# Kernel tuning notes

Hardware: AMD Instinct MI355X
Metric: run time of the kernel (lower is better)

The kernel has to match this reference:

```python
import jax, jax.numpy as jnp
import numpy as np

B, S, D, H, E, K = 8, 8192, 256, 1024, 8, 2


def setup_inputs() -> dict:
    key = jax.random.key(0)
    ks = jax.random.split(key, 7)
    s_in = 1.0 / np.sqrt(D)
    s_hid = 1.0 / np.sqrt(H)
    return {
        "x": jax.random.normal(ks[0], (B, S, D), dtype=jnp.float32),
        "Wg": jax.random.uniform(ks[1], (E, D), jnp.float32, -s_in, s_in),
        "bg": jax.random.uniform(ks[2], (E,), jnp.float32, -s_in, s_in),
        "W1": jax.random.uniform(ks[3], (E, H, D), jnp.float32, -s_in, s_in),
        "b1": jax.random.uniform(ks[4], (E, H), jnp.float32, -s_in, s_in),
        "W2": jax.random.uniform(ks[5], (E, D, H), jnp.float32, -s_hid, s_hid),
        "b2": jax.random.uniform(ks[6], (E, D), jnp.float32, -s_hid, s_hid),
    }


def reference(x, Wg, bg, W1, b1, W2, b2):
    # gate: [B,S,E]
    gate_scores = jnp.einsum("bsd,ed->bse", x, Wg) + bg
    topk_scores, topk_idx = jax.lax.top_k(gate_scores, K)  # [B,S,K]
    topk_probs = jax.nn.softmax(topk_scores, axis=-1)      # [B,S,K]
    # combine weight per expert: sum over top-k slots of prob * one_hot(idx)
    combine = jnp.sum(topk_probs[..., None] * jax.nn.one_hot(topk_idx, E, dtype=x.dtype), axis=-2)  # [B,S,E]
    out = jnp.zeros_like(x)
    for e in range(E):  # small fixed loop over experts
        h = jax.nn.relu(jnp.einsum("bsd,hd->bsh", x, W1[e]) + b1[e])
        y = jnp.einsum("bsh,dh->bsd", h, W2[e]) + b2[e]
        out = out + combine[..., e:e + 1] * y
    return out
```

## Files before the change

kernel.cpp:

```cpp
#include <hip/hip_runtime.h>
#include <hip/hip_bf16.h>

#define T_TOKENS 65536
#define D_DIM 256
#define H_DIM 1024
#define E_NUM 8
#define MT 128
#define HC 32
#define NCHUNK 32
#define GTB 64

typedef __attribute__((ext_vector_type(4))) float f32x4;
typedef __attribute__((ext_vector_type(8))) short s16x8;
typedef __attribute__((ext_vector_type(4))) unsigned int u32x4;
typedef __attribute__((ext_vector_type(4))) unsigned short u16x4;
typedef __attribute__((address_space(3))) unsigned int lds_u32;
typedef const __attribute__((address_space(1))) unsigned int glb_u32;

#define MFMA __builtin_amdgcn_mfma_f32_16x16x32_bf16

__device__ __forceinline__ unsigned short f2bf(float f){
  union { float f; unsigned u; } v; v.f = f;
  unsigned r = v.u + 0x7FFFu + ((v.u >> 16) & 1u);
  return (unsigned short)(r >> 16);
}
__device__ __forceinline__ float bf2f(unsigned short h){
  return __uint_as_float((unsigned)h << 16);
}
__device__ __forceinline__ unsigned cvtpk(float lo, float hi){
  unsigned r;
  asm("v_cvt_pk_bf16_f32 %0, %1, %2" : "=v"(r) : "v"(lo), "v"(hi));
  return r;
}
__device__ __forceinline__ unsigned long long pack4(f32x4 v){
  return (unsigned long long)f2bf(v.x)
       | ((unsigned long long)f2bf(v.y) << 16)
       | ((unsigned long long)f2bf(v.z) << 32)
       | ((unsigned long long)f2bf(v.w) << 48);
}

__device__ __forceinline__ void cvt_unit(int i, const float* __restrict__ W1,
                                         const float* __restrict__ W2,
                                         char* __restrict__ wsw){
  const int N1 = (E_NUM * H_DIM * D_DIM) / 4;
  unsigned long long pk;
  size_t off;
  if (i < N1){
    pk = pack4(((const f32x4*)W1)[i]);
    int idx = i << 2;
    int e  = idx >> 18;
    int h  = (idx >> 8) & (H_DIM - 1);
    int d0 = idx & (D_DIM - 1);
    int c = h >> 5, mi = (h >> 4) & 1, mrow = h & 15;
    int ks = d0 >> 5, qj = (d0 >> 3) & 3, e2 = d0 & 7;
    off = ((size_t)(e * NCHUNK + c) << 15)
        + (size_t)(((ks*2 + mi) << 10) + ((qj*16 + mrow) << 4) + (e2 << 1));
  } else {
    pk = pack4(((const f32x4*)W2)[i - N1]);
    int idx = (i - N1) << 2;
    int e   = idx >> 18;
    int d   = (idx >> 10) & (D_DIM - 1);
    int h0  = idx & (H_DIM - 1);
    int c   = h0 >> 5;
    int h32 = h0 & 31;
    int mi = (h32 >> 4) & 1, qj = (h32 >> 2) & 3;
    off = ((size_t)(e * NCHUNK + c) << 15) + 16384
        + (size_t)(((d >> 4) << 10) + ((qj * 16 + (d & 15)) << 4) + (mi << 3));
  }
  *(unsigned long long*)(wsw + off) = pk;
}

__global__ __launch_bounds__(256) void gate_kernel(
    const float* __restrict__ x, const float* __restrict__ Wg,
    const float* __restrict__ bg,
    const float* __restrict__ W1, const float* __restrict__ W2,
    char* __restrict__ wsw,
    int* __restrict__ counts, int* __restrict__ tok_ids, float* __restrict__ rrec)
{
  __shared__ int lcnt[E_NUM];
  __shared__ int lbase[E_NUM];
  __shared__ unsigned char aexp[GTB * 2];
  __shared__ short         apos[GTB * 2];

  int tid = threadIdx.x, wave = tid >> 6, lane = tid & 63;

  int gthr = blockIdx.x * 256 + tid;
#pragma unroll
  for (int j = 0; j < 4; ++j)
    cvt_unit(gthr + j * ((T_TOKENS / GTB) * 256), W1, W2, wsw);

  if (tid < E_NUM) lcnt[tid] = 0;
  __syncthreads();

  int t0 = blockIdx.x * GTB;
#pragma unroll 1
  for (int i = 0; i < GTB / 4; ++i){
    int tl = wave * (GTB / 4) + i;
    int t = t0 + tl;
    f32x4 xv = *(const f32x4*)(x + (size_t)t * D_DIM + 4*lane);
    float s[E_NUM];
#pragma unroll
    for (int e = 0; e < E_NUM; ++e){
      f32x4 w = *(const f32x4*)(Wg + e*D_DIM + 4*lane);
      s[e] = xv.x*w.x + xv.y*w.y + xv.z*w.z + xv.w*w.w;
    }
#pragma unroll
    for (int off = 32; off; off >>= 1){
#pragma unroll
      for (int e = 0; e < E_NUM; ++e) s[e] += __shfl_xor(s[e], off);
    }
#pragma unroll
    for (int e = 0; e < E_NUM; ++e) s[e] += bg[e];
    int e0 = 0; float v0 = s[0];
#pragma unroll
    for (int e = 1; e < E_NUM; ++e) if (s[e] > v0){ v0 = s[e]; e0 = e; }
    int e1 = -1; float v1 = -3.4e38f;
#pragma unroll
    for (int e = 0; e < E_NUM; ++e){
      if (e == e0) continue;
      if (s[e] > v1){ v1 = s[e]; e1 = e; }
    }
    float ex = __expf(v1 - v0);
    float inv = 1.f / (1.f + ex);
    float p0 = inv, p1 = ex * inv;
    if (lane == 0){
      int li = tl * 2;
      int pos0 = atomicAdd(&lcnt[e0], 1);
      int pos1 = atomicAdd(&lcnt[e1], 1);
      aexp[li]   = (unsigned char)e0; apos[li]   = (short)pos0;
      aexp[li+1] = (unsigned char)e1; apos[li+1] = (short)pos1;
      f32x4 rr; rr.x = p0; rr.y = p1; rr.z = (float)e0; rr.w = (float)e1;
      *(f32x4*)(rrec + (size_t)t * 4) = rr;
    }
  }
  __syncthreads();
  if (tid < E_NUM) lbase[tid] = atomicAdd(counts + tid*16, lcnt[tid]);
  __syncthreads();
  if (tid < GTB * 2){
    int t = t0 + (tid >> 1);
    int e = aexp[tid];
    int idx = lbase[e] + apos[tid];
    tok_ids[e*T_TOKENS + idx] = t | ((tid & 1) << 16);
  }
}

__global__ __launch_bounds__(256, 2) void ffn_kernel(
  const float* __restrict__ x, const char* __restrict__ wsw,
  const float* __restrict__ b1,
  const int* __restrict__ counts, const int* __restrict__ tok_ids,
  unsigned short* __restrict__ yslot)
{
  const int e    = blockIdx.x & 7;
  const int tile = blockIdx.x >> 3;
  const int cnt  = counts[e * 16];
  const int base = tile * MT;
  if (base >= cnt) return;

  __shared__ __align__(1024) unsigned short W1s[2][8192];
  __shared__ __align__(1024) unsigned short W2h[2][4096];
  __shared__ __align__(16)   float b1s[H_DIM];
  __shared__ int sTok[MT];

  const int tid = threadIdx.x, wave = tid >> 6, lane = tid & 63;
  const int mrow = lane & 15, qj = lane >> 4;
  const char* wexp = wsw + ((size_t)(e * NCHUNK) << 15);

  auto stage_w1 = [&](int c, int buf){
    const char* src = wexp + ((size_t)c << 15);
    char* dst = (char*)&W1s[buf][0];
#pragma unroll
    for (int i = 0; i < 4; ++i){
      int ub = i * 4096 + wave * 1024;
      __builtin_amdgcn_global_load_lds(
        (glb_u32*)(src + ub + lane * 16),
        (lds_u32*)(dst + ub), 16, 0, 0);
    }
  };
  auto stage_w2h = [&](int c, int buf){
    const char* src = wexp + ((size_t)c << 15) + 16384 + 8192;
    char* dst = (char*)&W2h[buf][0];
#pragma unroll
    for (int i = 0; i < 2; ++i){
      int ub = i * 4096 + wave * 1024;
      __builtin_amdgcn_global_load_lds(
        (glb_u32*)(src + ub + lane * 16),
        (lds_u32*)(dst + ub), 16, 0, 0);
    }
  };

  if (tid < MT){
    int idx = base + tid;
    sTok[tid] = (idx < cnt) ? tok_ids[e*T_TOKENS + idx] : -1;
  }
  *(f32x4*)&b1s[tid * 4] = ((const f32x4*)(b1 + e*H_DIM))[tid];
  __syncthreads();

  stage_w1(0, 0);
  stage_w2h(0, 0);

  s16x8 afr[2][8];
#pragma unroll
  for (int ti = 0; ti < 2; ++ti){
    int ent = sTok[wave*32 + ti*16 + mrow];
    int tk = ent & 0xFFFF;
    const f32x4* src = (const f32x4*)(x + (size_t)(ent < 0 ? 0 : tk) * D_DIM);
#pragma unroll
    for (int k = 0; k < 8; ++k){
      f32x4 a = src[k*8 + qj*2];
      f32x4 b = src[k*8 + qj*2 + 1];
      s16x8 f;
      f[0]=(short)f2bf(a.x); f[1]=(short)f2bf(a.y); f[2]=(short)f2bf(a.z); f[3]=(short)f2bf(a.w);
      f[4]=(short)f2bf(b.x); f[5]=(short)f2bf(b.y); f[6]=(short)f2bf(b.z); f[7]=(short)f2bf(b.w);
      if (ent < 0) f = (s16x8)(short)0;
      afr[ti][k] = f;
    }
  }

  const int lb = lane * 16;

  asm volatile("s_waitcnt vmcnt(0) lgkmcnt(0)" ::: "memory");
  __builtin_amdgcn_s_barrier();

  f32x4 yacc[16][2];
#pragma unroll
  for (int m = 0; m < 16; ++m){
    yacc[m][0] = (f32x4){0.f,0.f,0.f,0.f};
    yacc[m][1] = (f32x4){0.f,0.f,0.f,0.f};
  }

  int buf = 0;
#pragma unroll 1
  for (int c = 0; c < NCHUNK; ++c){
    if (c + 1 < NCHUNK){ stage_w1(c + 1, buf ^ 1); stage_w2h(c + 1, buf ^ 1); }

    const s16x8* w2g = (const s16x8*)(wexp + ((size_t)c << 15) + 16384) + lane;
    s16x8 g0 = w2g[0],   g1 = w2g[64],  g2 = w2g[128], g3 = w2g[192];
    s16x8 g4 = w2g[256], g5 = w2g[320], g6 = w2g[384], g7 = w2g[448];

    const char* Wb = (const char*)&W1s[buf][0];

    __builtin_amdgcn_s_setprio(1);
    f32x4 hacc[2][2];
    hacc[0][0] = (f32x4){0.f,0.f,0.f,0.f}; hacc[0][1] = (f32x4){0.f,0.f,0.f,0.f};
    hacc[1][0] = (f32x4){0.f,0.f,0.f,0.f}; hacc[1][1] = (f32x4){0.f,0.f,0.f,0.f};
#pragma unroll
    for (int ks = 0; ks < 8; ++ks){
      s16x8 wa = *(const s16x8*)(Wb + lb + (ks*2    )*1024);
      s16x8 wb = *(const s16x8*)(Wb + lb + (ks*2 + 1)*1024);
      hacc[0][0] = MFMA(wa, afr[0][ks], hacc[0][0], 0, 0, 0);
      hacc[0][1] = MFMA(wa, afr[1][ks], hacc[0][1], 0, 0, 0);
      hacc[1][0] = MFMA(wb, afr[0][ks], hacc[1][0], 0, 0, 0);
      hacc[1][1] = MFMA(wb, afr[1][ks], hacc[1][1], 0, 0, 0);
    }
    __builtin_amdgcn_s_setprio(0);

    f32x4 bv0 = *(const f32x4*)&b1s[c*32 + qj*4];
    f32x4 bv1 = *(const f32x4*)&b1s[c*32 + 16 + qj*4];
    s16x8 pb0, pb1;
    {
      f32x4 h0 = hacc[0][0], h1 = hacc[1][0];
      h0.x = fmaxf(h0.x + bv0.x, 0.f); h0.y = fmaxf(h0.y + bv0.y, 0.f);
      h0.z = fmaxf(h0.z + bv0.z, 0.f); h0.w = fmaxf(h0.w + bv0.w, 0.f);
      h1.x = fmaxf(h1.x + bv1.x, 0.f); h1.y = fmaxf(h1.y + bv1.y, 0.f);
      h1.z = fmaxf(h1.z + bv1.z, 0.f); h1.w = fmaxf(h1.w + bv1.w, 0.f);
      u32x4 pw;
      pw.x = cvtpk(h0.x, h0.y); pw.y = cvtpk(h0.z, h0.w);
      pw.z = cvtpk(h1.x, h1.y); pw.w = cvtpk(h1.z, h1.w);
      pb0 = __builtin_bit_cast(s16x8, pw);
    }
    {
      f32x4 h0 = hacc[0][1], h1 = hacc[1][1];
      h0.x = fmaxf(h0.x + bv0.x, 0.f); h0.y = fmaxf(h0.y + bv0.y, 0.f);
      h0.z = fmaxf(h0.z + bv0.z, 0.f); h0.w = fmaxf(h0.w + bv0.w, 0.f);
      h1.x = fmaxf(h1.x + bv1.x, 0.f); h1.y = fmaxf(h1.y + bv1.y, 0.f);
      h1.z = fmaxf(h1.z + bv1.z, 0.f); h1.w = fmaxf(h1.w + bv1.w, 0.f);
      u32x4 pw;
      pw.x = cvtpk(h0.x, h0.y); pw.y = cvtpk(h0.z, h0.w);
      pw.z = cvtpk(h1.x, h1.y); pw.w = cvtpk(h1.z, h1.w);
      pb1 = __builtin_bit_cast(s16x8, pw);
    }

    __builtin_amdgcn_s_setprio(1);
#define Y2(mm, ff) { yacc[mm][0] = MFMA(ff, pb0, yacc[mm][0], 0, 0, 0); \
                     yacc[mm][1] = MFMA(ff, pb1, yacc[mm][1], 0, 0, 0); }
    Y2(0, g0) Y2(1, g1) Y2(2, g2) Y2(3, g3)
    Y2(4, g4) Y2(5, g5) Y2(6, g6) Y2(7, g7)
    const char* Wl = (const char*)&W2h[buf][0];
#pragma unroll
    for (int m = 8; m < 16; ++m){
      s16x8 lf = *(const s16x8*)(Wl + lb + (m - 8)*1024);
      yacc[m][0] = MFMA(lf, pb0, yacc[m][0], 0, 0, 0);
      yacc[m][1] = MFMA(lf, pb1, yacc[m][1], 0, 0, 0);
    }
#undef Y2
    __builtin_amdgcn_s_setprio(0);

    asm volatile("s_waitcnt vmcnt(0) lgkmcnt(0)" ::: "memory");
    __builtin_amdgcn_s_barrier();
    buf ^= 1;
  }

#pragma unroll
  for (int ti = 0; ti < 2; ++ti){
    int ent = sTok[wave*32 + ti*16 + mrow];
    if (ent < 0) continue;
    int slot = ((ent & 0xFFFF) << 1) | ((ent >> 16) & 1);
    unsigned short* dst = yslot + (size_t)slot * 256;
#pragma unroll
    for (int m = 0; m < 16; ++m){
      unsigned lo = cvtpk(yacc[m][ti][0], yacc[m][ti][1]);
      unsigned hi = cvtpk(yacc[m][ti][2], yacc[m][ti][3]);
      *(unsigned*)(dst + m*16 + qj*4)     = lo;
      *(unsigned*)(dst + m*16 + qj*4 + 2) = hi;
    }
  }
}

__global__ __launch_bounds__(256) void combine_kernel(
    const float* __restrict__ rrec, const float* __restrict__ b2,
    float* __restrict__ out)
{
  int t = blockIdx.x * 4 + (threadIdx.x >> 6);
  int lane = threadIdx.x & 63;
  f32x4 rr = *(const f32x4*)(rrec + (size_t)t * 4);
  float p0 = rr.x, p1 = rr.y;
  int e0 = (int)rr.z, e1 = (int)rr.w;
  const u16x4* s0 = (const u16x4*)((const unsigned short*)out + (size_t)t * 512);
  u16x4 a = s0[lane];
  u16x4 b = s0[64 + lane];
  f32x4 z0 = *(const f32x4*)(b2 + e0*D_DIM + 4*lane);
  f32x4 z1 = *(const f32x4*)(b2 + e1*D_DIM + 4*lane);
  f32x4 o;
  o.x = p0*(bf2f(a.x) + z0.x) + p1*(bf2f(b.x) + z1.x);
  o.y = p0*(bf2f(a.y) + z0.y) + p1*(bf2f(b.y) + z1.y);
  o.z = p0*(bf2f(a.z) + z0.z) + p1*(bf2f(b.z) + z1.z);
  o.w = p0*(bf2f(a.w) + z0.w) + p1*(bf2f(b.w) + z1.w);
  *(f32x4*)(out + (size_t)t * D_DIM + 4*lane) = o;
}

extern "C" void kernel_launch(void* const* d_in, const int* in_sizes, int n_in,
                              void* d_out, int out_size, void* d_ws, size_t ws_size,
                              hipStream_t stream) {
  const float* x  = (const float*)d_in[0];
  const float* Wg = (const float*)d_in[1];
  const float* bg = (const float*)d_in[2];
  const float* W1 = (const float*)d_in[3];
  const float* b1 = (const float*)d_in[4];
  const float* W2 = (const float*)d_in[5];
  const float* b2 = (const float*)d_in[6];
  float* out = (float*)d_out;
  char* ws = (char*)d_ws;

  char*  wsw     = ws;
  int*   counts  = (int*)  (ws + 8388608);
  int*   tok_ids = (int*)  (ws + 8389632);
  float* rrec    = (float*)(ws + 10486784);

  hipMemsetAsync(counts, 0, 512, stream);
  gate_kernel<<<T_TOKENS/GTB, 256, 0, stream>>>(x, Wg, bg, W1, W2, wsw,
                                                counts, tok_ids, rrec);
  ffn_kernel<<<E_NUM * (T_TOKENS/MT), 256, 0, stream>>>(x, wsw, b1, counts, tok_ids,
                                                        (unsigned short*)d_out);
  combine_kernel<<<T_TOKENS/4, 256, 0, stream>>>(rrec, b2, out);
}
```

Before: 272.8 us.

## Double token tile to 256 with 512-thread blocks and stage full W2 chunk in LDS

```diff
diff --git a/kernel.cpp b/kernel.cpp
--- a/kernel.cpp
+++ b/kernel.cpp
@@ -5,7 +5,8 @@
 #define D_DIM 256
 #define H_DIM 1024
 #define E_NUM 8
-#define MT 128
+#define MT 256
+#define NTILE (T_TOKENS / MT)
 #define HC 32
 #define NCHUNK 32
 #define GTB 64
@@ -144,7 +145,7 @@
   }
 }
 
-__global__ __launch_bounds__(256, 2) void ffn_kernel(
+__global__ __launch_bounds__(512, 2) void ffn_kernel(
   const float* __restrict__ x, const char* __restrict__ wsw,
   const float* __restrict__ b1,
   const int* __restrict__ counts, const int* __restrict__ tok_ids,
@@ -156,8 +157,7 @@
   const int base = tile * MT;
   if (base >= cnt) return;
 
-  __shared__ __align__(1024) unsigned short W1s[2][8192];
-  __shared__ __align__(1024) unsigned short W2h[2][4096];
+  __shared__ __align__(1024) unsigned short Ws[2][16384];
   __shared__ __align__(16)   float b1s[H_DIM];
   __shared__ int sTok[MT];
 
@@ -165,38 +165,26 @@
   const int mrow = lane & 15, qj = lane >> 4;
   const char* wexp = wsw + ((size_t)(e * NCHUNK) << 15);
 
-  auto stage_w1 = [&](int c, int buf){
+  auto stage = [&](int c, int buf){
     const char* src = wexp + ((size_t)c << 15);
-    char* dst = (char*)&W1s[buf][0];
+    char* dst = (char*)&Ws[buf][0];
 #pragma unroll
     for (int i = 0; i < 4; ++i){
-      int ub = i * 4096 + wave * 1024;
+      int ub = i * 8192 + wave * 1024;
       __builtin_amdgcn_global_load_lds(
         (glb_u32*)(src + ub + lane * 16),
         (lds_u32*)(dst + ub), 16, 0, 0);
     }
   };
-  auto stage_w2h = [&](int c, int buf){
-    const char* src = wexp + ((size_t)c << 15) + 16384 + 8192;
-    char* dst = (char*)&W2h[buf][0];
-#pragma unroll
-    for (int i = 0; i < 2; ++i){
-      int ub = i * 4096 + wave * 1024;
-      __builtin_amdgcn_global_load_lds(
-        (glb_u32*)(src + ub + lane * 16),
-        (lds_u32*)(dst + ub), 16, 0, 0);
-    }
-  };
 
   if (tid < MT){
     int idx = base + tid;
     sTok[tid] = (idx < cnt) ? tok_ids[e*T_TOKENS + idx] : -1;
   }
-  *(f32x4*)&b1s[tid * 4] = ((const f32x4*)(b1 + e*H_DIM))[tid];
+  if (tid < 256) *(f32x4*)&b1s[tid * 4] = ((const f32x4*)(b1 + e*H_DIM))[tid];
   __syncthreads();
 
-  stage_w1(0, 0);
-  stage_w2h(0, 0);
+  stage(0, 0);
 
   s16x8 afr[2][8];
 #pragma unroll
@@ -231,13 +219,9 @@
   int buf = 0;
 #pragma unroll 1
   for (int c = 0; c < NCHUNK; ++c){
-    if (c + 1 < NCHUNK){ stage_w1(c + 1, buf ^ 1); stage_w2h(c + 1, buf ^ 1); }
-
-    const s16x8* w2g = (const s16x8*)(wexp + ((size_t)c << 15) + 16384) + lane;
-    s16x8 g0 = w2g[0],   g1 = w2g[64],  g2 = w2g[128], g3 = w2g[192];
-    s16x8 g4 = w2g[256], g5 = w2g[320], g6 = w2g[384], g7 = w2g[448];
-
-    const char* Wb = (const char*)&W1s[buf][0];
+    if (c + 1 < NCHUNK) stage(c + 1, buf ^ 1);
+
+    const char* Wb = (const char*)&Ws[buf][0];
 
     __builtin_amdgcn_s_setprio(1);
     f32x4 hacc[2][2];
@@ -281,18 +265,13 @@
     }
 
     __builtin_amdgcn_s_setprio(1);
-#define Y2(mm, ff) { yacc[mm][0] = MFMA(ff, pb0, yacc[mm][0], 0, 0, 0); \
-                     yacc[mm][1] = MFMA(ff, pb1, yacc[mm][1], 0, 0, 0); }
-    Y2(0, g0) Y2(1, g1) Y2(2, g2) Y2(3, g3)
-    Y2(4, g4) Y2(5, g5) Y2(6, g6) Y2(7, g7)
-    const char* Wl = (const char*)&W2h[buf][0];
-#pragma unroll
-    for (int m = 8; m < 16; ++m){
-      s16x8 lf = *(const s16x8*)(Wl + lb + (m - 8)*1024);
+    const char* Wl = Wb + 16384;
+#pragma unroll
+    for (int m = 0; m < 16; ++m){
+      s16x8 lf = *(const s16x8*)(Wl + lb + m*1024);
       yacc[m][0] = MFMA(lf, pb0, yacc[m][0], 0, 0, 0);
       yacc[m][1] = MFMA(lf, pb1, yacc[m][1], 0, 0, 0);
     }
-#undef Y2
     __builtin_amdgcn_s_setprio(0);
 
     asm volatile("s_waitcnt vmcnt(0) lgkmcnt(0)" ::: "memory");
@@ -359,7 +338,7 @@
   hipMemsetAsync(counts, 0, 512, stream);
   gate_kernel<<<T_TOKENS/GTB, 256, 0, stream>>>(x, Wg, bg, W1, W2, wsw,
                                                 counts, tok_ids, rrec);
-  ffn_kernel<<<E_NUM * (T_TOKENS/MT), 256, 0, stream>>>(x, wsw, b1, counts, tok_ids,
-                                                        (unsigned short*)d_out);
+  ffn_kernel<<<E_NUM * NTILE, 512, 0, stream>>>(x, wsw, b1, counts, tok_ids,
+                                                (unsigned short*)d_out);
   combine_kernel<<<T_TOKENS/4, 256, 0, stream>>>(rrec, b2, out);
 }
```

Result: slower. 296.4 us (+8.6%).
